# Performance work log

Measured on AMD Instinct MI355X. Metric: run time of the kernel, lower is better.

Reference implementation:

```python
import jax, jax.numpy as jnp
import numpy as np


def setup_inputs() -> dict:
    key = jax.random.key(0)
    k1, k2, k3 = jax.random.split(key, 3)
    B, M, J = 4096, 64, 24  # batch, n_max_markers, n_joints
    points = jax.random.normal(k1, (B, M, 3), dtype=jnp.float32)
    weight = jax.random.uniform(k2, (B, M, J), dtype=jnp.float32)  # positive soft weights
    offset = jax.random.normal(k3, (B, M, J, 3), dtype=jnp.float32)
    return {"points": points, "weight": weight, "offset": offset}


def reference(points, weight, offset):
    # P: per-joint marker offsets (B, J, 3, M); Q: world marker positions (B, 1, 3, M)
    P = jnp.transpose(offset, (0, 2, 3, 1))
    Q = jnp.transpose(points, (0, 2, 1))[:, None]
    w = jnp.transpose(weight, (0, 2, 1))[:, :, None]  # (B, J, 1, M)

    wsum = jnp.sum(w, axis=-1)                   # (B, J, 1)
    P_ = jnp.sum(P * w, axis=-1) / wsum          # (B, J, 3) weighted centroid of offsets
    Q_ = jnp.sum(Q * w, axis=-1) / wsum          # (B, J, 3) weighted centroid of markers

    X = P - P_[..., None]                        # (B, J, 3, M)
    Y = Q - Q_[..., None]                        # (B, J, 3, M) via broadcast

    # Cross-covariance S = X @ Y^T (NOTE: original multiplies un-weighted centered coords)
    S = jnp.einsum('bjdm,bjem->bjde', X, Y)      # (B, J, 3, 3)

    U, _, Vh = jnp.linalg.svd(S)
    V = jnp.swapaxes(Vh, -1, -2)
    Ut = jnp.swapaxes(U, -1, -2)
    det = jnp.linalg.det(jnp.matmul(V, Ut))      # (B, J) reflection correction
    Ut = Ut.at[..., -1, :].multiply(det[..., None])
    R = jnp.matmul(V, Ut)                        # (B, J, 3, 3) optimal rotation
    t = Q_[..., None] - jnp.matmul(R, P_[..., None])  # (B, J, 3, 1)
    return R, t
```

## Files before the change

### kernel.cpp

```cpp
#include <hip/hip_runtime.h>


constexpr int M = 64;
constexpr int J = 24;
constexpr int NACC = 22;
constexpr int NWS  = 15;
constexpr int KSP  = 8;
constexpr int SPW  = 8;
constexpr int SPB  = 32;

__global__ __launch_bounds__(256, 6) void accum_kernel(
    const float* __restrict__ points,
    const float* __restrict__ weight,
    const float* __restrict__ offset,
    float* __restrict__ ws,
    int bj_total)
{
    const int t    = threadIdx.x;
    const int lane = t & 63;
    const int wv   = t >> 6;
    const int k    = lane >> 3;
    const int sl   = lane & 7;
    const int bj   = blockIdx.x * SPB + wv * SPW + sl;
    const int bjc  = bj < bj_total ? bj : bj_total - 1;
    const int b    = bjc / J;
    const int j    = bjc - b * J;

    const float* wq = weight + (size_t)b * (M * J) + (size_t)(k * 8) * J + j;
    const float* oq = offset + ((size_t)b * (M * J) + (size_t)(k * 8) * J + j) * 3;
    const float* pq = points + (size_t)b * (M * 3) + (size_t)(k * 8) * 3;

    float acc[NACC];
#pragma unroll
    for (int n = 0; n < NACC; ++n) acc[n] = 0.0f;

#pragma unroll
    for (int i = 0; i < M / KSP; ++i) {
        float w  = wq[i * J];
        float o0 = oq[i * (J * 3) + 0];
        float o1 = oq[i * (J * 3) + 1];
        float o2 = oq[i * (J * 3) + 2];
        float p0 = pq[i * 3 + 0];
        float p1 = pq[i * 3 + 1];
        float p2 = pq[i * 3 + 2];
        acc[0] += w;
        acc[1] = fmaf(w, o0, acc[1]);  acc[2] = fmaf(w, o1, acc[2]);  acc[3] = fmaf(w, o2, acc[3]);
        acc[4] = fmaf(w, p0, acc[4]);  acc[5] = fmaf(w, p1, acc[5]);  acc[6] = fmaf(w, p2, acc[6]);
        acc[7] += o0; acc[8] += o1; acc[9] += o2;
        acc[10] += p0; acc[11] += p1; acc[12] += p2;
        acc[13] = fmaf(o0, p0, acc[13]); acc[14] = fmaf(o0, p1, acc[14]); acc[15] = fmaf(o0, p2, acc[15]);
        acc[16] = fmaf(o1, p0, acc[16]); acc[17] = fmaf(o1, p1, acc[17]); acc[18] = fmaf(o1, p2, acc[18]);
        acc[19] = fmaf(o2, p0, acc[19]); acc[20] = fmaf(o2, p1, acc[20]); acc[21] = fmaf(o2, p2, acc[21]);
    }

#pragma unroll
    for (int n = 0; n < NACC; ++n) {
        float v = acc[n];
        v += __shfl_xor(v, 8);
        v += __shfl_xor(v, 16);
        v += __shfl_xor(v, 32);
        acc[n] = v;
    }

    if (k != 0 || bj >= bj_total) return;

    const float inv = __builtin_amdgcn_rcpf(acc[0]);
    const float cP0 = acc[1] * inv, cP1 = acc[2] * inv, cP2 = acc[3] * inv;
    const float cQ0 = acc[4] * inv, cQ1 = acc[5] * inv, cQ2 = acc[6] * inv;
    const float To0 = acc[7], To1 = acc[8], To2 = acc[9];
    const float Tp0 = acc[10], Tp1 = acc[11], Tp2 = acc[12];
    const float fM = (float)M;
    float Sv[NWS];
    Sv[0] = acc[13] - cP0 * Tp0 - cQ0 * To0 + fM * cP0 * cQ0;
    Sv[1] = acc[14] - cP0 * Tp1 - cQ1 * To0 + fM * cP0 * cQ1;
    Sv[2] = acc[15] - cP0 * Tp2 - cQ2 * To0 + fM * cP0 * cQ2;
    Sv[3] = acc[16] - cP1 * Tp0 - cQ0 * To1 + fM * cP1 * cQ0;
    Sv[4] = acc[17] - cP1 * Tp1 - cQ1 * To1 + fM * cP1 * cQ1;
    Sv[5] = acc[18] - cP1 * Tp2 - cQ2 * To1 + fM * cP1 * cQ2;
    Sv[6] = acc[19] - cP2 * Tp0 - cQ0 * To2 + fM * cP2 * cQ0;
    Sv[7] = acc[20] - cP2 * Tp1 - cQ1 * To2 + fM * cP2 * cQ1;
    Sv[8] = acc[21] - cP2 * Tp2 - cQ2 * To2 + fM * cP2 * cQ2;
    Sv[9]  = cP0; Sv[10] = cP1; Sv[11] = cP2;
    Sv[12] = cQ0; Sv[13] = cQ1; Sv[14] = cQ2;
#pragma unroll
    for (int n = 0; n < NWS; ++n) ws[(size_t)n * bj_total + bj] = Sv[n];
}

template<int P, int Q>
__device__ __forceinline__ void jrot(float A[4][4], float V[4][4]) {
    float apq = A[P][Q];
    float theta = (A[Q][Q] - A[P][P]) * __builtin_amdgcn_rcpf(2.0f * apq);
    float t = __builtin_amdgcn_rcpf(fabsf(theta) + __builtin_amdgcn_sqrtf(fmaf(theta, theta, 1.0f)));
    t = (theta < 0.0f) ? -t : t;
    t = (apq == 0.0f) ? 0.0f : t;
    float c = __builtin_amdgcn_rsqf(fmaf(t, t, 1.0f));
    float s = t * c;
#pragma unroll
    for (int k = 0; k < 4; ++k) {
        float akp = A[k][P], akq = A[k][Q];
        A[k][P] = c * akp - s * akq;
        A[k][Q] = s * akp + c * akq;
    }
#pragma unroll
    for (int k = 0; k < 4; ++k) {
        float apk = A[P][k], aqk = A[Q][k];
        A[P][k] = c * apk - s * aqk;
        A[Q][k] = s * apk + c * aqk;
        float vkp = V[k][P], vkq = V[k][Q];
        V[k][P] = c * vkp - s * vkq;
        V[k][Q] = s * vkp + c * vkq;
    }
}

__device__ __forceinline__ void horn_solve(
    float S00, float S01, float S02, float S10, float S11, float S12,
    float S20, float S21, float S22,
    float cP0, float cP1, float cP2, float cQ0, float cQ1, float cQ2,
    float* __restrict__ Rout, float* __restrict__ tout)
{
    float A[4][4], V[4][4];
    A[0][0] = S00 + S11 + S22;
    A[0][1] = A[1][0] = S12 - S21;
    A[0][2] = A[2][0] = S20 - S02;
    A[0][3] = A[3][0] = S01 - S10;
    A[1][1] = S00 - S11 - S22;
    A[1][2] = A[2][1] = S01 + S10;
    A[1][3] = A[3][1] = S02 + S20;
    A[2][2] = -S00 + S11 - S22;
    A[2][3] = A[3][2] = S12 + S21;
    A[3][3] = -S00 - S11 + S22;
#pragma unroll
    for (int r = 0; r < 4; ++r)
#pragma unroll
        for (int c = 0; c < 4; ++c)
            V[r][c] = (r == c) ? 1.0f : 0.0f;

#pragma unroll 1
    for (int sweep = 0; sweep < 6; ++sweep) {
        jrot<0, 1>(A, V); jrot<0, 2>(A, V); jrot<0, 3>(A, V);
        jrot<1, 2>(A, V); jrot<1, 3>(A, V); jrot<2, 3>(A, V);
    }

    float best = A[0][0];
    float qw = V[0][0], qx = V[1][0], qy = V[2][0], qz = V[3][0];
#pragma unroll
    for (int i = 1; i < 4; ++i) {
        bool better = A[i][i] > best;
        best = better ? A[i][i] : best;
        qw = better ? V[0][i] : qw;
        qx = better ? V[1][i] : qx;
        qy = better ? V[2][i] : qy;
        qz = better ? V[3][i] : qz;
    }
    float nrm = __builtin_amdgcn_rsqf(qw * qw + qx * qx + qy * qy + qz * qz);
    qw *= nrm; qx *= nrm; qy *= nrm; qz *= nrm;

    float R00 = 1.f - 2.f * (qy * qy + qz * qz);
    float R01 = 2.f * (qx * qy - qw * qz);
    float R02 = 2.f * (qx * qz + qw * qy);
    float R10 = 2.f * (qx * qy + qw * qz);
    float R11 = 1.f - 2.f * (qx * qx + qz * qz);
    float R12 = 2.f * (qy * qz - qw * qx);
    float R20 = 2.f * (qx * qz - qw * qy);
    float R21 = 2.f * (qy * qz + qw * qx);
    float R22 = 1.f - 2.f * (qx * qx + qy * qy);

    Rout[0] = R00; Rout[1] = R01; Rout[2] = R02;
    Rout[3] = R10; Rout[4] = R11; Rout[5] = R12;
    Rout[6] = R20; Rout[7] = R21; Rout[8] = R22;
    tout[0] = cQ0 - (R00 * cP0 + R01 * cP1 + R02 * cP2);
    tout[1] = cQ1 - (R10 * cP0 + R11 * cP1 + R12 * cP2);
    tout[2] = cQ2 - (R20 * cP0 + R21 * cP1 + R22 * cP2);
}

__global__ __launch_bounds__(64) void solve_kernel(
    const float* __restrict__ ws, float* __restrict__ out, int bj_total)
{
    int tid = blockIdx.x * 64 + threadIdx.x;
    if (tid >= bj_total) return;
    float Sv[NWS];
#pragma unroll
    for (int n = 0; n < NWS; ++n) Sv[n] = ws[(size_t)n * bj_total + tid];
    float Rr[9], tr[3];
    horn_solve(Sv[0], Sv[1], Sv[2], Sv[3], Sv[4], Sv[5], Sv[6], Sv[7], Sv[8],
               Sv[9], Sv[10], Sv[11], Sv[12], Sv[13], Sv[14], Rr, tr);
    float* Rout = out + (size_t)tid * 9;
#pragma unroll
    for (int n = 0; n < 9; ++n) Rout[n] = Rr[n];
    float* tout = out + (size_t)bj_total * 9 + (size_t)tid * 3;
    tout[0] = tr[0]; tout[1] = tr[1]; tout[2] = tr[2];
}

__global__ __launch_bounds__(256) void fused_kernel(
    const float* __restrict__ points, const float* __restrict__ weight,
    const float* __restrict__ offset, float* __restrict__ out, int bj_total)
{
    int tid = blockIdx.x * blockDim.x + threadIdx.x;
    if (tid >= bj_total) return;
    int b = tid / J, j = tid - b * J;
    const float* wq = weight + (size_t)b * M * J + j;
    const float* oq = offset + ((size_t)b * M * J + j) * 3;
    const float* pq = points + (size_t)b * M * 3;
    float a[NACC];
#pragma unroll
    for (int n = 0; n < NACC; ++n) a[n] = 0.0f;
#pragma unroll 4
    for (int m = 0; m < M; ++m) {
        float w = wq[m * J];
        float o0 = oq[m * (J * 3) + 0], o1 = oq[m * (J * 3) + 1], o2 = oq[m * (J * 3) + 2];
        float p0 = pq[m * 3 + 0], p1 = pq[m * 3 + 1], p2 = pq[m * 3 + 2];
        a[0] += w;
        a[1] = fmaf(w, o0, a[1]); a[2] = fmaf(w, o1, a[2]); a[3] = fmaf(w, o2, a[3]);
        a[4] = fmaf(w, p0, a[4]); a[5] = fmaf(w, p1, a[5]); a[6] = fmaf(w, p2, a[6]);
        a[7] += o0; a[8] += o1; a[9] += o2;
        a[10] += p0; a[11] += p1; a[12] += p2;
        a[13] = fmaf(o0, p0, a[13]); a[14] = fmaf(o0, p1, a[14]); a[15] = fmaf(o0, p2, a[15]);
        a[16] = fmaf(o1, p0, a[16]); a[17] = fmaf(o1, p1, a[17]); a[18] = fmaf(o1, p2, a[18]);
        a[19] = fmaf(o2, p0, a[19]); a[20] = fmaf(o2, p1, a[20]); a[21] = fmaf(o2, p2, a[21]);
    }
    float inv = __builtin_amdgcn_rcpf(a[0]);
    float cP0 = a[1] * inv, cP1 = a[2] * inv, cP2 = a[3] * inv;
    float cQ0 = a[4] * inv, cQ1 = a[5] * inv, cQ2 = a[6] * inv;
    const float fM = (float)M;
    float S00 = a[13] - cP0 * a[10] - cQ0 * a[7] + fM * cP0 * cQ0;
    float S01 = a[14] - cP0 * a[11] - cQ1 * a[7] + fM * cP0 * cQ1;
    float S02 = a[15] - cP0 * a[12] - cQ2 * a[7] + fM * cP0 * cQ2;
    float S10 = a[16] - cP1 * a[10] - cQ0 * a[8] + fM * cP1 * cQ0;
    float S11 = a[17] - cP1 * a[11] - cQ1 * a[8] + fM * cP1 * cQ1;
    float S12 = a[18] - cP1 * a[12] - cQ2 * a[8] + fM * cP1 * cQ2;
    float S20 = a[19] - cP2 * a[10] - cQ0 * a[9] + fM * cP2 * cQ0;
    float S21 = a[20] - cP2 * a[11] - cQ1 * a[9] + fM * cP2 * cQ1;
    float S22 = a[21] - cP2 * a[12] - cQ2 * a[9] + fM * cP2 * cQ2;
    float Rr[9], tr[3];
    horn_solve(S00, S01, S02, S10, S11, S12, S20, S21, S22,
               cP0, cP1, cP2, cQ0, cQ1, cQ2, Rr, tr);
    float* Rout = out + (size_t)tid * 9;
#pragma unroll
    for (int n = 0; n < 9; ++n) Rout[n] = Rr[n];
    float* tout = out + (size_t)bj_total * 9 + (size_t)tid * 3;
    tout[0] = tr[0]; tout[1] = tr[1]; tout[2] = tr[2];
}

extern "C" void kernel_launch(void* const* d_in, const int* in_sizes, int n_in,
                              void* d_out, int out_size, void* d_ws, size_t ws_size,
                              hipStream_t stream) {
    const float* points = (const float*)d_in[0];
    const float* weight = (const float*)d_in[1];
    const float* offset = (const float*)d_in[2];
    float* out = (float*)d_out;

    int B = in_sizes[0] / (M * 3);
    int bj_total = B * J;

    size_t need = (size_t)NWS * bj_total * sizeof(float);
    if (ws_size >= need) {
        int grid1 = (bj_total + SPB - 1) / SPB;
        accum_kernel<<<grid1, 256, 0, stream>>>(points, weight, offset, (float*)d_ws, bj_total);
        solve_kernel<<<(bj_total + 63) / 64, 64, 0, stream>>>((const float*)d_ws, out, bj_total);
    } else {
        fused_kernel<<<(bj_total + 255) / 256, 256, 0, stream>>>(points, weight, offset, out, bj_total);
    }
}
```

Measured before the change: 147.4 us.

## Stage each batch's inputs in LDS with coalesced float4 loads in accum kernel

```diff
diff --git a/kernel.cpp b/kernel.cpp
--- a/kernel.cpp
+++ b/kernel.cpp
@@ -5,44 +5,73 @@
 constexpr int J = 24;
 constexpr int NACC = 22;
 constexpr int NWS  = 15;
-constexpr int KSP  = 8;
-constexpr int SPW  = 8;
-constexpr int SPB  = 32;
-
-__global__ __launch_bounds__(256, 6) void accum_kernel(
+
+constexpr int L4_W = 0;
+constexpr int L4_O = 384;
+constexpr int L4_P = 1536;
+constexpr int L4_N = 1584;
+
+__global__ __launch_bounds__(256, 4) void accum_kernel(
     const float* __restrict__ points,
     const float* __restrict__ weight,
     const float* __restrict__ offset,
     float* __restrict__ ws,
     int bj_total)
 {
-    const int t    = threadIdx.x;
+    const int b = blockIdx.x;
+    const int t = threadIdx.x;
+
+    __shared__ float4 lds4[L4_N];
+
+    const float4* wb4 = (const float4*)(weight + (size_t)b * (M * J));
+    const float4* ob4 = (const float4*)(offset + (size_t)b * (M * J * 3));
+    const float4* pb4 = (const float4*)(points + (size_t)b * (M * 3));
+
+    float4 o0_ = ob4[t];
+    float4 o1_ = ob4[t + 256];
+    float4 o2_ = ob4[t + 512];
+    float4 o3_ = ob4[t + 768];
+    float4 w0_ = wb4[t];
+    float4 o4_ = {0.f, 0.f, 0.f, 0.f};
+    float4 w1_ = {0.f, 0.f, 0.f, 0.f};
+    float4 p0_ = {0.f, 0.f, 0.f, 0.f};
+    if (t < 128) { o4_ = ob4[1024 + t]; w1_ = wb4[256 + t]; }
+    if (t < 48)  { p0_ = pb4[t]; }
+
+    lds4[L4_O + t]        = o0_;
+    lds4[L4_O + 256 + t]  = o1_;
+    lds4[L4_O + 512 + t]  = o2_;
+    lds4[L4_O + 768 + t]  = o3_;
+    lds4[L4_W + t]        = w0_;
+    if (t < 128) { lds4[L4_O + 1024 + t] = o4_; lds4[L4_W + 256 + t] = w1_; }
+    if (t < 48)  { lds4[L4_P + t] = p0_; }
+
+    __syncthreads();
+
     const int lane = t & 63;
     const int wv   = t >> 6;
-    const int k    = lane >> 3;
-    const int sl   = lane & 7;
-    const int bj   = blockIdx.x * SPB + wv * SPW + sl;
-    const int bjc  = bj < bj_total ? bj : bj_total - 1;
-    const int b    = bjc / J;
-    const int j    = bjc - b * J;
-
-    const float* wq = weight + (size_t)b * (M * J) + (size_t)(k * 8) * J + j;
-    const float* oq = offset + ((size_t)b * (M * J) + (size_t)(k * 8) * J + j) * 3;
-    const float* pq = points + (size_t)b * (M * 3) + (size_t)(k * 8) * 3;
+    const int kk   = lane & 7;
+    const int jj   = (lane >> 3) + wv * 8;
+    if (jj >= J) return;
+
+    const float* w_s = (const float*)lds4;
+    const float* o_s = (const float*)lds4 + 4 * L4_O;
+    const float* p_s = (const float*)lds4 + 4 * L4_P;
 
     float acc[NACC];
 #pragma unroll
     for (int n = 0; n < NACC; ++n) acc[n] = 0.0f;
 
 #pragma unroll
-    for (int i = 0; i < M / KSP; ++i) {
-        float w  = wq[i * J];
-        float o0 = oq[i * (J * 3) + 0];
-        float o1 = oq[i * (J * 3) + 1];
-        float o2 = oq[i * (J * 3) + 2];
-        float p0 = pq[i * 3 + 0];
-        float p1 = pq[i * 3 + 1];
-        float p2 = pq[i * 3 + 2];
+    for (int i = 0; i < M / 8; ++i) {
+        const int m = i * 8 + kk;
+        float w  = w_s[m * J + jj];
+        float o0 = o_s[m * 72 + jj * 3 + 0];
+        float o1 = o_s[m * 72 + jj * 3 + 1];
+        float o2 = o_s[m * 72 + jj * 3 + 2];
+        float p0 = p_s[m * 3 + 0];
+        float p1 = p_s[m * 3 + 1];
+        float p2 = p_s[m * 3 + 2];
         acc[0] += w;
         acc[1] = fmaf(w, o0, acc[1]);  acc[2] = fmaf(w, o1, acc[2]);  acc[3] = fmaf(w, o2, acc[3]);
         acc[4] = fmaf(w, p0, acc[4]);  acc[5] = fmaf(w, p1, acc[5]);  acc[6] = fmaf(w, p2, acc[6]);
@@ -56,13 +85,13 @@
 #pragma unroll
     for (int n = 0; n < NACC; ++n) {
         float v = acc[n];
-        v += __shfl_xor(v, 8);
-        v += __shfl_xor(v, 16);
-        v += __shfl_xor(v, 32);
+        v += __shfl_xor(v, 1);
+        v += __shfl_xor(v, 2);
+        v += __shfl_xor(v, 4);
         acc[n] = v;
     }
 
-    if (k != 0 || bj >= bj_total) return;
+    if (kk != 0) return;
 
     const float inv = __builtin_amdgcn_rcpf(acc[0]);
     const float cP0 = acc[1] * inv, cP1 = acc[2] * inv, cP2 = acc[3] * inv;
@@ -82,6 +111,8 @@
     Sv[8] = acc[21] - cP2 * Tp2 - cQ2 * To2 + fM * cP2 * cQ2;
     Sv[9]  = cP0; Sv[10] = cP1; Sv[11] = cP2;
     Sv[12] = cQ0; Sv[13] = cQ1; Sv[14] = cQ2;
+
+    const int bj = b * J + jj;
 #pragma unroll
     for (int n = 0; n < NWS; ++n) ws[(size_t)n * bj_total + bj] = Sv[n];
 }
@@ -254,8 +285,7 @@
 
     size_t need = (size_t)NWS * bj_total * sizeof(float);
     if (ws_size >= need) {
-        int grid1 = (bj_total + SPB - 1) / SPB;
-        accum_kernel<<<grid1, 256, 0, stream>>>(points, weight, offset, (float*)d_ws, bj_total);
+        accum_kernel<<<B, 256, 0, stream>>>(points, weight, offset, (float*)d_ws, bj_total);
         solve_kernel<<<(bj_total + 63) / 64, 64, 0, stream>>>((const float*)d_ws, out, bj_total);
     } else {
         fused_kernel<<<(bj_total + 255) / 256, 256, 0, stream>>>(points, weight, offset, out, bj_total);
```

Result: no change. 147.7 us (+0.2%).
